# Performance work log

Measured on AMD Instinct MI355X. Metric: run time of the kernel, lower is better.

The kernel has to match this reference:

```python
import jax, jax.numpy as jnp
import numpy as np

EMBED_DIM = 768
NUM_HEADS = 12
FF_DIM = 3072
HEAD_DIM = EMBED_DIM // NUM_HEADS
LN_EPS = 1e-5


def setup_inputs() -> dict:
    key = jax.random.key(0)
    ks = jax.random.split(key, 10)
    C, F = EMBED_DIM, FF_DIM
    s = lambda d: 1.0 / np.sqrt(d)
    return {
        "x": jax.random.normal(ks[0], (2, 2048, C), dtype=jnp.float32),
        "w_qkv": jax.random.normal(ks[1], (C, 3 * C), dtype=jnp.float32) * s(C),
        "w_out": jax.random.normal(ks[2], (C, C), dtype=jnp.float32) * s(C),
        "ln1_g": jnp.ones((C,), jnp.float32),
        "ln1_b": jnp.zeros((C,), jnp.float32),
        "ln2_g": jnp.ones((C,), jnp.float32),
        "ln2_b": jnp.zeros((C,), jnp.float32),
        "w1": jax.random.normal(ks[3], (C, F), dtype=jnp.float32) * s(C),
        "b1": jnp.zeros((F,), jnp.float32),
        "w2": jax.random.normal(ks[4], (F, C), dtype=jnp.float32) * s(F),
        "b2": jnp.zeros((C,), jnp.float32),
    }


def _layernorm(x, g, b):
    mu = jnp.mean(x, axis=-1, keepdims=True)
    var = jnp.var(x, axis=-1, keepdims=True)
    return (x - mu) * jax.lax.rsqrt(var + LN_EPS) * g + b


def _attention(x, w_qkv, w_out):
    B, T, C = x.shape
    qkv = x @ w_qkv                               # [B,T,3C]
    q, k, v = jnp.split(qkv, 3, axis=2)
    def heads(t):  # [B,T,C] -> [B,H,T,Dh]
        return t.reshape(B, T, NUM_HEADS, HEAD_DIM).transpose(0, 2, 1, 3)
    q, k, v = heads(q), heads(k), heads(v)
    att = jnp.einsum("bhqd,bhkd->bhqk", q, k) / np.sqrt(HEAD_DIM)
    mask = jnp.tril(jnp.ones((T, T), bool))
    att = jnp.where(mask, att, -jnp.inf)
    att = jax.nn.softmax(att, axis=-1)
    out = jnp.einsum("bhqk,bhkd->bhqd", att, v)   # [B,H,T,Dh]
    out = out.transpose(0, 2, 1, 3).reshape(B, T, C)
    return out @ w_out


def reference(x, w_qkv, w_out, ln1_g, ln1_b, ln2_g, ln2_b, w1, b1, w2, b2):
    x = x + _attention(_layernorm(x, ln1_g, ln1_b), w_qkv, w_out)
    h = _layernorm(x, ln2_g, ln2_b)
    h = jax.nn.gelu(h @ w1 + b1, approximate=False) @ w2 + b2
    return x + h
```

## Files before the change

kernel.cpp:

```cpp
#include <hip/hip_runtime.h>
#include <hip/hip_bf16.h>
#include <math.h>

typedef __attribute__((ext_vector_type(8))) short short8;
typedef __attribute__((ext_vector_type(4))) float f32x4;
typedef __attribute__((address_space(1))) const void CG;
typedef __attribute__((address_space(3))) void LS;

#define LOAD_LDS16(src, dst) __builtin_amdgcn_global_load_lds((CG*)(src), (LS*)(dst), 16, 0, 0)

__device__ __forceinline__ short f2bf(float f) {
  union { float f; unsigned u; } v; v.f = f;
  unsigned r = v.u + 0x7fffu + ((v.u >> 16) & 1u);
  return (short)(r >> 16);
}

__global__ __launch_bounds__(256) void transp_all(const float* __restrict__ w_qkv,
                                                  const float* __restrict__ w_out,
                                                  const float* __restrict__ w1,
                                                  const float* __restrict__ w2,
                                                  short* __restrict__ wqkvT,
                                                  short* __restrict__ woutT,
                                                  short* __restrict__ w1T,
                                                  short* __restrict__ w2T) {
  __shared__ short t[32][33];
  int bid = blockIdx.x;
  const float* W; short* Wt; int K, N, nx, id;
  if (bid < 1728)      { W = w_qkv; Wt = wqkvT; K = 768;  N = 2304; nx = 72; id = bid; }
  else if (bid < 2304) { W = w_out; Wt = woutT; K = 768;  N = 768;  nx = 24; id = bid - 1728; }
  else if (bid < 4608) { W = w1;    Wt = w1T;   K = 768;  N = 3072; nx = 96; id = bid - 2304; }
  else                 { W = w2;    Wt = w2T;   K = 3072; N = 768;  nx = 24; id = bid - 4608; }
  int n0 = (id % nx) << 5, k0 = (id / nx) << 5;
  int tid = threadIdx.x;
#pragma unroll
  for (int p = 0; p < 4; ++p) {
    int e = tid + (p << 8);
    int r = e >> 5, c = e & 31;
    t[r][c] = f2bf(W[(size_t)(k0 + r) * N + n0 + c]);
  }
  __syncthreads();
#pragma unroll
  for (int p = 0; p < 4; ++p) {
    int e = tid + (p << 8);
    int r = e >> 5, c = e & 31;
    Wt[(size_t)(n0 + r) * K + k0 + c] = t[c][r];
  }
}

__global__ __launch_bounds__(256) void ln_kernel(const float* __restrict__ x,
                                                 const float* __restrict__ g,
                                                 const float* __restrict__ b,
                                                 short* __restrict__ out) {
  int row = blockIdx.x;
  const float* xr = x + (size_t)row * 768;
  int tid = threadIdx.x;
  float v0 = xr[tid], v1 = xr[tid + 256], v2 = xr[tid + 512];
  float s = v0 + v1 + v2;
  float ss = v0 * v0 + v1 * v1 + v2 * v2;
#pragma unroll
  for (int m = 1; m < 64; m <<= 1) { s += __shfl_xor(s, m); ss += __shfl_xor(ss, m); }
  __shared__ float red[8];
  int w = tid >> 6;
  if ((tid & 63) == 0) { red[w] = s; red[w + 4] = ss; }
  __syncthreads();
  s = red[0] + red[1] + red[2] + red[3];
  ss = red[4] + red[5] + red[6] + red[7];
  float mean = s * (1.0f / 768.0f);
  float var = ss * (1.0f / 768.0f) - mean * mean;
  float rs = rsqrtf(var + 1e-5f);
  short* outr = out + (size_t)row * 768;
  outr[tid]       = f2bf((v0 - mean) * rs * g[tid]       + b[tid]);
  outr[tid + 256] = f2bf((v1 - mean) * rs * g[tid + 256] + b[tid + 256]);
  outr[tid + 512] = f2bf((v2 - mean) * rs * g[tid + 512] + b[tid + 512]);
}

template <int EPI>
__global__ __launch_bounds__(256, 2) void gemm_bt(
    const short* __restrict__ A, const short* __restrict__ Bt,
    int M, int N, int K,
    short* __restrict__ outQ, short* __restrict__ outK, short* __restrict__ outVt,
    float* __restrict__ outF, short* __restrict__ outB,
    const float* __restrict__ bias, const float* __restrict__ resid) {
  __shared__ short lA[128 * 32];
  __shared__ short lB[128 * 32];
  int tid = threadIdx.x;
  int lane = tid & 63, w = tid >> 6;
  int li = lane & 15, g = lane >> 4;
  int bm = blockIdx.y << 7, bn = blockIdx.x << 7;
  int wrow = (w >> 1) << 6, wcol = (w & 1) << 6;
  size_t lda = (EPI == 4) ? 3072 : (size_t)K;
  int koff = (EPI == 4) ? (int)blockIdx.z * 1536 : 0;

  const short* as[2];
  const short* bs[2];
#pragma unroll
  for (int p = 0; p < 2; ++p) {
    int v = tid + (p << 8);
    int row = v >> 2;
    int lc = (v & 3) ^ ((row ^ (row >> 2)) & 3);
    as[p] = A + (size_t)(bm + row) * lda + koff + lc * 8;
    bs[p] = Bt + (size_t)(bn + row) * lda + koff + lc * 8;
  }
  char* lAb = (char*)lA;
  char* lBb = (char*)lB;
  int sg = (g ^ ((li ^ (li >> 2)) & 3)) << 3;

  f32x4 zero = {0.f, 0.f, 0.f, 0.f};
  f32x4 acc[4][4];
#pragma unroll
  for (int i = 0; i < 4; ++i)
#pragma unroll
    for (int j = 0; j < 4; ++j) acc[i][j] = zero;

  for (int k0 = 0; k0 < K; k0 += 32) {
    __syncthreads();
#pragma unroll
    for (int p = 0; p < 2; ++p) {
      LOAD_LDS16(as[p] + k0, lAb + (p << 12) + (w << 10));
      LOAD_LDS16(bs[p] + k0, lBb + (p << 12) + (w << 10));
    }
    __syncthreads();
    short8 af[4], bf[4];
#pragma unroll
    for (int rt = 0; rt < 4; ++rt)
      af[rt] = *(const short8*)&lA[(wrow + rt * 16 + li) * 32 + sg];
#pragma unroll
    for (int ct = 0; ct < 4; ++ct)
      bf[ct] = *(const short8*)&lB[(wcol + ct * 16 + li) * 32 + sg];
#pragma unroll
    for (int rt = 0; rt < 4; ++rt)
#pragma unroll
      for (int ct = 0; ct < 4; ++ct)
        acc[rt][ct] = __builtin_amdgcn_mfma_f32_16x16x32_bf16(af[rt], bf[ct], acc[rt][ct], 0, 0, 0);
  }

#pragma unroll
  for (int rt = 0; rt < 4; ++rt) {
    int mbase = bm + wrow + rt * 16 + g * 4;
#pragma unroll
    for (int ct = 0; ct < 4; ++ct) {
      int n = bn + wcol + ct * 16 + li;
      f32x4 c = acc[rt][ct];
      if (EPI == 0) {
        if (n < 768) {
          int h = n >> 6, d = n & 63;
#pragma unroll
          for (int i = 0; i < 4; ++i) {
            int tok = mbase + i;
            int bb = tok >> 11, t = tok & 2047;
            outQ[((size_t)((bb * 12 + h) * 2048 + t) << 6) + d] = f2bf(c[i]);
          }
        } else if (n < 1536) {
          int nn = n - 768;
          int h = nn >> 6, d = nn & 63;
#pragma unroll
          for (int i = 0; i < 4; ++i) {
            int tok = mbase + i;
            int bb = tok >> 11, t = tok & 2047;
            outK[((size_t)((bb * 12 + h) * 2048 + t) << 6) + d] = f2bf(c[i]);
          }
        } else {
          int nn = n - 1536;
          int h = nn >> 6, d = nn & 63;
          int bb = mbase >> 11, t = mbase & 2047;
          ushort4 pk;
          pk.x = (unsigned short)f2bf(c[0]);
          pk.y = (unsigned short)f2bf(c[1]);
          pk.z = (unsigned short)f2bf(c[2]);
          pk.w = (unsigned short)f2bf(c[3]);
          *(ushort4*)((unsigned short*)outVt + (((size_t)((bb * 12 + h) * 64 + d)) << 11) + t) = pk;
        }
      } else if (EPI == 1) {
#pragma unroll
        for (int i = 0; i < 4; ++i) {
          int m = mbase + i;
          outF[(size_t)m * N + n] = c[i] + resid[(size_t)m * N + n];
        }
      } else if (EPI == 2) {
        float bv = bias[n];
#pragma unroll
        for (int i = 0; i < 4; ++i) {
          int m = mbase + i;
          float xx = c[i] + bv;
          float gel = 0.5f * xx * (1.0f + erff(xx * 0.70710678118654752f));
          outB[(size_t)m * N + n] = f2bf(gel);
        }
      } else if (EPI == 3) {
        float bv = bias[n];
#pragma unroll
        for (int i = 0; i < 4; ++i) {
          int m = mbase + i;
          outF[(size_t)m * N + n] = c[i] + bv + resid[(size_t)m * N + n];
        }
      } else {
        bool last = (blockIdx.z == 1);
        float bv = last ? bias[n] : 0.f;
#pragma unroll
        for (int i = 0; i < 4; ++i) {
          int m = mbase + i;
          float add = c[i] + bv + (last ? resid[(size_t)m * N + n] : 0.f);
          atomicAdd(&outF[(size_t)m * N + n], add);
        }
      }
    }
  }
}

__global__ __launch_bounds__(256, 3) void attn_kernel(const short* __restrict__ Q,
                                                      const short* __restrict__ Kk,
                                                      const short* __restrict__ Vt,
                                                      unsigned short* __restrict__ o_part,
                                                      float* __restrict__ ml_part) {
  __shared__ short lK[2][64 * 64];
  __shared__ short lV[2][64 * 64];
  __shared__ short lP[4][32 * 64];
  int tid = threadIdx.x;
  int lane = tid & 63, w = tid >> 6;
  int li = lane & 15, g = lane >> 4;
  int bh = blockIdx.y;
  int cid = 39 - (int)blockIdx.x;
  int qt = 0, cum = 0;
  while (true) { int n = (qt >> 2) + 1; if (cid < cum + n) break; cum += n; ++qt; }
  int c = cid - cum;
  int nch = (qt >> 2) + 1;
  int nt = (qt + 1) << 1;
  int bq = nt / nch, rem = nt % nch;
  int t0 = c * bq + (c < rem ? c : rem);
  int t1 = t0 + bq + (c < rem ? 1 : 0);

  int qbase = (qt << 7) + (w << 5);
  const short* Qb = Q + ((size_t)bh << 17);
  const short* Kb = Kk + ((size_t)bh << 17);
  const short* Vb = Vt + ((size_t)bh << 17);

  short8 qf[2][2];
#pragma unroll
  for (int rt = 0; rt < 2; ++rt)
#pragma unroll
    for (int kc = 0; kc < 2; ++kc)
      qf[rt][kc] = *(const short8*)&Qb[(size_t)(qbase + rt * 16 + li) * 64 + kc * 32 + g * 8];

  int r0 = tid >> 3, s0 = (tid & 7) ^ (r0 & 7);
  int r1 = r0 + 32,  s1 = (tid & 7) ^ (r1 & 7);
  const short* kS0 = Kb + r0 * 64 + s0 * 8;
  const short* kS1 = Kb + r1 * 64 + s1 * 8;
  const short* vS0 = Vb + (size_t)r0 * 2048 + s0 * 8;
  const short* vS1 = Vb + (size_t)r1 * 2048 + s1 * 8;

#define STAGE(buf, kt)                                                        \
  do {                                                                        \
    LOAD_LDS16(kS0 + (size_t)(kt) * 4096, (char*)lK[buf] + (w << 10));        \
    LOAD_LDS16(kS1 + (size_t)(kt) * 4096, (char*)lK[buf] + 4096 + (w << 10)); \
    LOAD_LDS16(vS0 + (size_t)(kt) * 64,   (char*)lV[buf] + (w << 10));        \
    LOAD_LDS16(vS1 + (size_t)(kt) * 64,   (char*)lV[buf] + 4096 + (w << 10)); \
  } while (0)

  const short8 kOnes = {0x3F80, 0x3F80, 0x3F80, 0x3F80, 0x3F80, 0x3F80, 0x3F80, 0x3F80};
  f32x4 zero = {0.f, 0.f, 0.f, 0.f};
  f32x4 o[2][4];
  f32x4 lrow[2];
  float mrow[2] = {-1e30f, -1e30f};
#pragma unroll
  for (int rt = 0; rt < 2; ++rt) {
    lrow[rt] = zero;
#pragma unroll
    for (int ct = 0; ct < 4; ++ct) o[rt][ct] = zero;
  }

  int diagKt = qbase >> 6;
  const float SCALE = 0.18033688011112042f;
  int sw = li & 7;
  unsigned short* Pw = (unsigned short*)lP[w];

  STAGE(0, t0);

  for (int kt = t0; kt < t1; ++kt) {
    int cur = (kt - t0) & 1;
    __syncthreads();
    if (kt + 1 < t1) STAGE(cur ^ 1, kt + 1);

    if (kt <= diagKt) {
      const short* Kc = lK[cur];
      const short* Vc = lV[cur];

      f32x4 s[2][4];
#pragma unroll
      for (int rt = 0; rt < 2; ++rt)
#pragma unroll
        for (int ct = 0; ct < 4; ++ct) s[rt][ct] = zero;
#pragma unroll
      for (int kc = 0; kc < 2; ++kc)
#pragma unroll
        for (int ct = 0; ct < 4; ++ct) {
          short8 kf = *(const short8*)&Kc[(ct * 16 + li) * 64 + ((((kc << 2) | g) ^ sw) << 3)];
#pragma unroll
          for (int rt = 0; rt < 2; ++rt)
            s[rt][ct] = __builtin_amdgcn_mfma_f32_16x16x32_bf16(qf[rt][kc], kf, s[rt][ct], 0, 0, 0);
        }

      if (kt == diagKt) {
        int kb0 = kt << 6;
#pragma unroll
        for (int rt = 0; rt < 2; ++rt) {
          int qrow0 = qbase + rt * 16 + g * 4;
#pragma unroll
          for (int ct = 0; ct < 4; ++ct) {
            int kcol = kb0 + ct * 16 + li;
#pragma unroll
            for (int i = 0; i < 4; ++i)
              if (kcol > qrow0 + i) s[rt][ct][i] = -1e30f;
          }
        }
      }

#pragma unroll
      for (int rt = 0; rt < 2; ++rt) {
        float tm = s[rt][0][0];
#pragma unroll
        for (int ct = 0; ct < 4; ++ct)
#pragma unroll
          for (int i = 0; i < 4; ++i) tm = fmaxf(tm, s[rt][ct][i]);
#pragma unroll
        for (int m2 = 1; m2 < 64; m2 <<= 1) tm = fmaxf(tm, __shfl_xor(tm, m2));
        if (tm > mrow[rt] + 8.0f) {
          float corr = exp2f((mrow[rt] - tm) * SCALE);
          mrow[rt] = tm;
#pragma unroll
          for (int i = 0; i < 4; ++i) lrow[rt][i] *= corr;
#pragma unroll
          for (int ct = 0; ct < 4; ++ct)
#pragma unroll
            for (int i = 0; i < 4; ++i) o[rt][ct][i] *= corr;
        }
#pragma unroll
        for (int ct = 0; ct < 4; ++ct)
#pragma unroll
          for (int i = 0; i < 4; ++i) {
            float p = exp2f((s[rt][ct][i] - mrow[rt]) * SCALE);
            int row = rt * 16 + (g << 2) + i;
            int col = (ct << 4) + li;
            int ch = (col >> 3) ^ (row & 7);
            Pw[(row << 6) + (ch << 3) + (col & 7)] = (unsigned short)f2bf(p);
          }
      }

      f32x4 psum[2];
      psum[0] = zero; psum[1] = zero;
#pragma unroll
      for (int kc = 0; kc < 2; ++kc) {
        short8 vf[4];
#pragma unroll
        for (int ct = 0; ct < 4; ++ct)
          vf[ct] = *(const short8*)&Vc[(ct * 16 + li) * 64 + ((((kc << 2) | g) ^ sw) << 3)];
#pragma unroll
        for (int rt = 0; rt < 2; ++rt) {
          short8 pf = *(const short8*)&lP[w][(rt * 16 + li) * 64 + ((((kc << 2) | g) ^ sw) << 3)];
#pragma unroll
          for (int ct = 0; ct < 4; ++ct)
            o[rt][ct] = __builtin_amdgcn_mfma_f32_16x16x32_bf16(pf, vf[ct], o[rt][ct], 0, 0, 0);
          psum[rt] = __builtin_amdgcn_mfma_f32_16x16x32_bf16(pf, kOnes, psum[rt], 0, 0, 0);
        }
      }
#pragma unroll
      for (int rt = 0; rt < 2; ++rt)
#pragma unroll
        for (int i = 0; i < 4; ++i) lrow[rt][i] += psum[rt][i];
    }
  }
#undef STAGE

  int pid = bh * 40 + cid;
#pragma unroll
  for (int rt = 0; rt < 2; ++rt)
#pragma unroll
    for (int ct = 0; ct < 4; ++ct) {
      int col = (ct << 4) + li;
      int row0 = (w << 5) + (rt << 4) + (g << 2);
      ushort4 pk;
      pk.x = (unsigned short)f2bf(o[rt][ct][0]);
      pk.y = (unsigned short)f2bf(o[rt][ct][1]);
      pk.z = (unsigned short)f2bf(o[rt][ct][2]);
      pk.w = (unsigned short)f2bf(o[rt][ct][3]);
      *(ushort4*)&o_part[((size_t)pid * 64 + col) * 128 + row0] = pk;
    }
  if (li == 0) {
    float2* mlp = (float2*)ml_part;
#pragma unroll
    for (int rt = 0; rt < 2; ++rt)
#pragma unroll
      for (int i = 0; i < 4; ++i) {
        int row = (w << 5) + (rt << 4) + (g << 2) + i;
        mlp[(size_t)pid * 128 + row] = make_float2(mrow[rt], lrow[rt][i]);
      }
  }
}

__global__ __launch_bounds__(256) void attn_combine(const unsigned short* __restrict__ o_part,
                                                    const float* __restrict__ ml_part,
                                                    short* __restrict__ O) {
  __shared__ float wgt[4][128];
  int qt = blockIdx.x, bh = blockIdx.y;
  int a = qt >> 2, bb = qt & 3;
  int c0 = 2 * a * (a - 1) + a * bb + qt;
  int nch = a + 1;
  int pid0 = bh * 40 + c0;
  int tid = threadIdx.x;
  const float SCALE = 0.18033688011112042f;
  const float2* mlp = (const float2*)ml_part;

  if (tid < 128) {
    int row = tid;
    float mv[4] = {-1e30f, -1e30f, -1e30f, -1e30f};
    float lv[4] = {0.f, 0.f, 0.f, 0.f};
#pragma unroll
    for (int c = 0; c < 4; ++c)
      if (c < nch) {
        float2 ml = mlp[(size_t)(pid0 + c) * 128 + row];
        mv[c] = ml.x; lv[c] = ml.y;
      }
    float M = fmaxf(fmaxf(mv[0], mv[1]), fmaxf(mv[2], mv[3]));
    float u[4];
    float L = 0.f;
#pragma unroll
    for (int c = 0; c < 4; ++c) {
      u[c] = (c < nch) ? exp2f((mv[c] - M) * SCALE) : 0.f;
      L += lv[c] * u[c];
    }
    float inv = 1.0f / L;
#pragma unroll
    for (int c = 0; c < 4; ++c) wgt[c][row] = u[c] * inv;
  }
  __syncthreads();

  int col = tid & 63, rg = tid >> 6;
  int b = bh / 12, h = bh % 12;
  size_t obase[4];
#pragma unroll
  for (int c = 0; c < 4; ++c) obase[c] = ((size_t)(pid0 + c) * 64 + col) * 128;
  for (int r = 0; r < 32; ++r) {
    int row = (rg << 5) + r;
    float acc = 0.f;
#pragma unroll
    for (int c = 0; c < 4; ++c)
      if (c < nch) {
        union { unsigned u; float f; } cv;
        cv.u = ((unsigned)o_part[obase[c] + row]) << 16;
        acc += cv.f * wgt[c][row];
      }
    int t = (qt << 7) + row;
    O[((size_t)(b * 2048 + t)) * 768 + h * 64 + col] = f2bf(acc);
  }
}

extern "C" void kernel_launch(void* const* d_in, const int* in_sizes, int n_in,
                              void* d_out, int out_size, void* d_ws, size_t ws_size,
                              hipStream_t stream) {
  const float* x     = (const float*)d_in[0];
  const float* w_qkv = (const float*)d_in[1];
  const float* w_out = (const float*)d_in[2];
  const float* ln1g  = (const float*)d_in[3];
  const float* ln1b  = (const float*)d_in[4];
  const float* ln2g  = (const float*)d_in[5];
  const float* ln2b  = (const float*)d_in[6];
  const float* w1    = (const float*)d_in[7];
  const float* b1    = (const float*)d_in[8];
  const float* w2    = (const float*)d_in[9];
  const float* b2    = (const float*)d_in[10];
  float* out = (float*)d_out;
  char* ws = (char*)d_ws;

  short* wqkvT = (short*)(ws + 0);
  short* woutT = (short*)(ws + 3538944);
  short* w1T   = (short*)(ws + 4718592);
  short* w2T   = (short*)(ws + 9437184);
  short* qb    = (short*)(ws + 14155776);
  short* kb    = (short*)(ws + 20447232);
  short* vtb   = (short*)(ws + 26738688);
  short* attnb = (short*)(ws + 33030144);
  short* ab    = qb;
  short* xnb   = (short*)(ws + 39321600);
  float* x2b   = (float*)(ws + 45613056);
  unsigned short* o_part = (unsigned short*)(ws + 39321600);
  float* ml_part = (float*)(ws + 55050240);

  transp_all<<<dim3(6912), 256, 0, stream>>>(w_qkv, w_out, w1, w2, wqkvT, woutT, w1T, w2T);

  ln_kernel<<<dim3(4096), 256, 0, stream>>>(x, ln1g, ln1b, xnb);

  gemm_bt<0><<<dim3(18, 32), 256, 0, stream>>>(xnb, wqkvT, 4096, 2304, 768,
                                               qb, kb, vtb, nullptr, nullptr, nullptr, nullptr);

  attn_kernel<<<dim3(40, 24), 256, 0, stream>>>(qb, kb, vtb, o_part, ml_part);
  attn_combine<<<dim3(16, 24), 256, 0, stream>>>(o_part, ml_part, attnb);

  gemm_bt<1><<<dim3(6, 32), 256, 0, stream>>>(attnb, woutT, 4096, 768, 768,
                                              nullptr, nullptr, nullptr, x2b, nullptr, nullptr, x);

  ln_kernel<<<dim3(4096), 256, 0, stream>>>(x2b, ln2g, ln2b, xnb);

  gemm_bt<2><<<dim3(24, 32), 256, 0, stream>>>(xnb, w1T, 4096, 3072, 768,
                                               nullptr, nullptr, nullptr, nullptr, ab, b1, nullptr);

  hipMemsetAsync(out, 0, (size_t)4096 * 768 * 4, stream);
  gemm_bt<4><<<dim3(6, 32, 2), 256, 0, stream>>>(ab, w2T, 4096, 768, 1536,
                                                 nullptr, nullptr, nullptr, out, nullptr, b2, x2b);
}
```

Before: 255.9 us.

## Double-buffer GEMM LDS tiles and remap workgroups for XCD and L2 locality

Splits the GEMM's LDS tiles into two buffers so the global-to-LDS load of the next K-slice is issued before the MFMAs on the current slice, removing one barrier per iteration and overlapping memory with compute. Also remaps workgroup IDs, first spreading them across the 8 XCDs and then ordering them in groups of 8 row tiles, to improve L2 reuse of A and B tiles. The cost is twice the LDS per block, which may reduce occupancy. The remap also assumes the grid size divides evenly by 8.

```diff
diff --git a/kernel.cpp b/kernel.cpp
--- a/kernel.cpp
+++ b/kernel.cpp
@@ -81,12 +81,25 @@
     short* __restrict__ outQ, short* __restrict__ outK, short* __restrict__ outVt,
     float* __restrict__ outF, short* __restrict__ outB,
     const float* __restrict__ bias, const float* __restrict__ resid) {
-  __shared__ short lA[128 * 32];
-  __shared__ short lB[128 * 32];
+  __shared__ short lA[2][128 * 32];
+  __shared__ short lB[2][128 * 32];
   int tid = threadIdx.x;
   int lane = tid & 63, w = tid >> 6;
   int li = lane & 15, g = lane >> 4;
-  int bm = blockIdx.y << 7, bn = blockIdx.x << 7;
+
+  int nx = gridDim.x, ny = gridDim.y;
+  int nwg = nx * ny;
+  int fid = (int)blockIdx.y * nx + (int)blockIdx.x;
+  int nid = (fid & 7) * (nwg >> 3) + (fid >> 3);
+  const int GM = 8;
+  int npg = GM * nx;
+  int grp = nid / npg;
+  int fm = grp * GM;
+  int gs = min(GM, ny - fm);
+  int lid = nid - grp * npg;
+  int bm = (fm + lid % gs) << 7;
+  int bn = (lid / gs) << 7;
+
   int wrow = (w >> 1) << 6, wcol = (w & 1) << 6;
   size_t lda = (EPI == 4) ? 3072 : (size_t)K;
   int koff = (EPI == 4) ? (int)blockIdx.z * 1536 : 0;
@@ -101,8 +114,6 @@
     as[p] = A + (size_t)(bm + row) * lda + koff + lc * 8;
     bs[p] = Bt + (size_t)(bn + row) * lda + koff + lc * 8;
   }
-  char* lAb = (char*)lA;
-  char* lBb = (char*)lB;
   int sg = (g ^ ((li ^ (li >> 2)) & 3)) << 3;
 
   f32x4 zero = {0.f, 0.f, 0.f, 0.f};
@@ -112,27 +123,37 @@
 #pragma unroll
     for (int j = 0; j < 4; ++j) acc[i][j] = zero;
 
-  for (int k0 = 0; k0 < K; k0 += 32) {
+#define GSTAGE(buf, ki)                                                 \
+  do {                                                                  \
+    int kk = (ki) << 5;                                                 \
+    LOAD_LDS16(as[0] + kk, (char*)lA[buf] + (w << 10));                 \
+    LOAD_LDS16(as[1] + kk, (char*)lA[buf] + 4096 + (w << 10));          \
+    LOAD_LDS16(bs[0] + kk, (char*)lB[buf] + (w << 10));                 \
+    LOAD_LDS16(bs[1] + kk, (char*)lB[buf] + 4096 + (w << 10));          \
+  } while (0)
+
+  int nk = K >> 5;
+  GSTAGE(0, 0);
+  for (int ki = 0; ki < nk; ++ki) {
+    int cur = ki & 1;
     __syncthreads();
-#pragma unroll
-    for (int p = 0; p < 2; ++p) {
-      LOAD_LDS16(as[p] + k0, lAb + (p << 12) + (w << 10));
-      LOAD_LDS16(bs[p] + k0, lBb + (p << 12) + (w << 10));
-    }
-    __syncthreads();
+    if (ki + 1 < nk) GSTAGE(cur ^ 1, ki + 1);
+    const short* lAc = lA[cur];
+    const short* lBc = lB[cur];
     short8 af[4], bf[4];
 #pragma unroll
     for (int rt = 0; rt < 4; ++rt)
-      af[rt] = *(const short8*)&lA[(wrow + rt * 16 + li) * 32 + sg];
+      af[rt] = *(const short8*)&lAc[(wrow + rt * 16 + li) * 32 + sg];
 #pragma unroll
     for (int ct = 0; ct < 4; ++ct)
-      bf[ct] = *(const short8*)&lB[(wcol + ct * 16 + li) * 32 + sg];
+      bf[ct] = *(const short8*)&lBc[(wcol + ct * 16 + li) * 32 + sg];
 #pragma unroll
     for (int rt = 0; rt < 4; ++rt)
 #pragma unroll
       for (int ct = 0; ct < 4; ++ct)
         acc[rt][ct] = __builtin_amdgcn_mfma_f32_16x16x32_bf16(af[rt], bf[ct], acc[rt][ct], 0, 0, 0);
   }
+#undef GSTAGE
 
 #pragma unroll
   for (int rt = 0; rt < 4; ++rt) {
```

After: 243.8 us. 4.7% less time.
